# Performance work log

Hardware: AMD Instinct MI355X
Metric: run time of the kernel (lower is better)

Reference implementation:

```python
import jax, jax.numpy as jnp
import numpy as np

B, H, W, C, WS, NH = 32, 56, 56, 384, 7, 12
HD = C // NH            # head dim = 32
HID = 4 * C             # mlp hidden = 1536
SCALE = HD ** -0.5
EPS = 1e-5


def setup_inputs() -> dict:
    key = jax.random.key(0)
    ks = jax.random.split(key, 12)
    w = lambda k, shape: jax.random.normal(k, shape, jnp.float32) * 0.02
    return {
        "x": jax.random.normal(ks[0], (B, H * W, C), jnp.float32),
        "ln1_w": jnp.ones((C,), jnp.float32),
        "ln1_b": jnp.zeros((C,), jnp.float32),
        "qkv_w": w(ks[1], (3 * C, C)),          # nn.Linear weight [out,in], no bias
        "proj_w": w(ks[2], (C, C)),
        "proj_b": jnp.zeros((C,), jnp.float32),
        "ln2_w": jnp.ones((C,), jnp.float32),
        "ln2_b": jnp.zeros((C,), jnp.float32),
        "fc1_w": w(ks[3], (HID, C)),
        "fc1_b": jnp.zeros((HID,), jnp.float32),
        "fc2_w": w(ks[4], (C, HID)),
        "fc2_b": jnp.zeros((C,), jnp.float32),
    }


def _layer_norm(x, w, b):
    mu = jnp.mean(x, axis=-1, keepdims=True)
    var = jnp.mean((x - mu) ** 2, axis=-1, keepdims=True)
    return (x - mu) * jax.lax.rsqrt(var + EPS) * w + b


def _window_partition(x):
    # x: [B, H, W, C] -> [B*nW, WS*WS, C]
    x = x.reshape(B, H // WS, WS, W // WS, WS, C)
    x = x.transpose(0, 1, 3, 2, 4, 5)
    return x.reshape(-1, WS * WS, C)


def _window_reverse(xw):
    # [B*nW, WS*WS, C] -> [B, H*W, C]
    x = xw.reshape(B, H // WS, W // WS, WS, WS, C)
    x = x.transpose(0, 1, 3, 2, 4, 5)
    return x.reshape(B, H * W, C)


def reference(x, ln1_w, ln1_b, qkv_w, proj_w, proj_b, ln2_w, ln2_b,
              fc1_w, fc1_b, fc2_w, fc2_b):
    h = x
    xn = _layer_norm(x, ln1_w, ln1_b)
    xw = _window_partition(xn.reshape(B, H, W, C))      # [nB, N, C], N = 49

    # windowed multi-head self-attention
    qkv = xw @ qkv_w.T                                  # [nB, N, 3C]
    q, k, v = jnp.split(qkv, 3, axis=-1)
    def heads(t):
        return t.reshape(t.shape[0], t.shape[1], NH, HD).transpose(0, 2, 1, 3)
    q, k, v = heads(q), heads(k), heads(v)              # [nB, NH, N, HD]
    attn = jnp.einsum('bhnd,bhmd->bhnm', q, k) * SCALE
    attn = jax.nn.softmax(attn, axis=-1)
    out = jnp.einsum('bhnm,bhmd->bhnd', attn, v)        # [nB, NH, N, HD]
    out = out.transpose(0, 2, 1, 3).reshape(xw.shape[0], WS * WS, C)
    out = out @ proj_w.T + proj_b

    x = h + _window_reverse(out)

    # MLP (note: GELU applied after both fc1 and fc2, as in source)
    h = x
    xn = _layer_norm(x, ln2_w, ln2_b)
    y = jax.nn.gelu(xn @ fc1_w.T + fc1_b, approximate=False)
    y = jax.nn.gelu(y @ fc2_w.T + fc2_b, approximate=False)
    return h + y
```

## Files before the change

kernel.cpp:

```cpp
#include <hip/hip_runtime.h>
#include <cstdint>

#define TOKENS 100352
#define CDIM 384
#define HIDDIM 1536
#define NQKV 1152
#define NHEAD 12
#define NWIN_ALL 2048

typedef __bf16 bf16x8 __attribute__((ext_vector_type(8)));
typedef float f32x4 __attribute__((ext_vector_type(4)));
typedef unsigned short u16;
typedef u16 u16x8 __attribute__((ext_vector_type(8)));

typedef __attribute__((address_space(1))) unsigned int u32_as1;
typedef __attribute__((address_space(3))) unsigned int u32_as3;

__device__ __forceinline__ float bf2f(u16 u) {
    union { unsigned int i; float f; } v; v.i = ((unsigned int)u) << 16; return v.f;
}
__device__ __forceinline__ u16 f2bf(float f) {
    union { float f; unsigned int i; } v; v.f = f;
    unsigned int i = v.i;
    i += 0x7fffu + ((i >> 16) & 1u);
    return (u16)(i >> 16);
}
__device__ __forceinline__ float gelu_f(float x) {
    const float u = x * (0.7978845608028654f + 0.035677408136300125f * x * x);
    const float a = __builtin_fabsf(u);
    const float e = __expf(2.0f * a);
    float t = 1.0f - 2.0f * __builtin_amdgcn_rcpf(e + 1.0f);
    t = __builtin_copysignf(t, u);
    return 0.5f * x * (1.0f + t);
}
__device__ __forceinline__ void gload16(const u16* g, u16* l) {
    __builtin_amdgcn_global_load_lds((const u32_as1*)g, (u32_as3*)l, 16, 0, 0);
}

__global__ void cvt_kernel(const float* __restrict__ in, u16* __restrict__ out, int n) {
    int i = blockIdx.x * blockDim.x + threadIdx.x;
    if (i < n) out[i] = f2bf(in[i]);
}

__global__ __launch_bounds__(256) void ln_kernel(const float* __restrict__ x,
                                                 const float* __restrict__ w,
                                                 const float* __restrict__ b,
                                                 u16* __restrict__ out) {
    const int wid = threadIdx.x >> 6, lane = threadIdx.x & 63;
    const long row = (long)blockIdx.x * 4 + wid;
    const float* xr = x + row * CDIM;
    float v[6];
#pragma unroll
    for (int i = 0; i < 6; i++) v[i] = xr[lane + i * 64];
    float s = 0.f;
#pragma unroll
    for (int i = 0; i < 6; i++) s += v[i];
#pragma unroll
    for (int off = 32; off >= 1; off >>= 1) s += __shfl_xor(s, off, 64);
    const float mu = s * (1.0f / CDIM);
    float q = 0.f;
#pragma unroll
    for (int i = 0; i < 6; i++) { float d = v[i] - mu; q += d * d; }
#pragma unroll
    for (int off = 32; off >= 1; off >>= 1) q += __shfl_xor(q, off, 64);
    const float rs = rsqrtf(q * (1.0f / CDIM) + 1e-5f);
    u16* orow = out + row * CDIM;
#pragma unroll
    for (int i = 0; i < 6; i++) {
        const int c = lane + i * 64;
        orow[c] = f2bf((v[i] - mu) * rs * w[c] + b[c]);
    }
}

template <int EPI>
__global__ __launch_bounds__(256, 2) void gemm_kernel(const u16* __restrict__ A,
                                                      const u16* __restrict__ Bw,
                                                      const float* __restrict__ bias,
                                                      const float* __restrict__ res,
                                                      void* __restrict__ outp,
                                                      int N, int K) {
    __shared__ u16 lsA0[128 * 64];
    __shared__ u16 lsB0[128 * 64];
    __shared__ u16 lsA1[128 * 64];
    __shared__ u16 lsB1[128 * 64];
    const int ntiles = N >> 7;
    const int nwg = gridDim.x;
    const int bid = blockIdx.x;
    const int wg = ((nwg & 7) == 0) ? ((bid & 7) * (nwg >> 3) + (bid >> 3)) : bid;
    const int tm = wg / ntiles, tn = wg % ntiles;
    const int tid = threadIdx.x, wid = tid >> 6, lane = tid & 63;
    const int wr = wid >> 1, wc = wid & 1;

    const int srow = wid * 32 + (lane >> 3);
    const int schunk = (lane & 7) ^ (lane >> 3);
    const u16* gA = A + (size_t)(tm * 128 + srow) * K + schunk * 8;
    const u16* gB = Bw + (size_t)(tn * 128 + srow) * K + schunk * 8;
    const size_t rskip = (size_t)8 * K;
    const int lofs = wid * 2048;

    f32x4 acc[4][4] = {};

    const int rA = wr * 64 + (lane & 15);
    const int rB = wc * 64 + (lane & 15);
    const int ksub = lane >> 4;
    const int rx = lane & 7;

    auto STAGE = [&](u16* la, u16* lb, int kofs) {
#pragma unroll
        for (int j = 0; j < 4; j++) {
            gload16(gA + kofs + j * rskip, la + lofs + j * 512);
            gload16(gB + kofs + j * rskip, lb + lofs + j * 512);
        }
    };
    auto COMPUTE = [&](const u16* la, const u16* lb) {
#pragma unroll
        for (int kk = 0; kk < 2; kk++) {
            const int ca = (((kk << 2) + ksub) ^ rx) << 3;
            bf16x8 af[4], bfr[4];
#pragma unroll
            for (int mi = 0; mi < 4; mi++)
                af[mi] = *(const bf16x8*)(la + (rA + mi * 16) * 64 + ca);
#pragma unroll
            for (int ni = 0; ni < 4; ni++)
                bfr[ni] = *(const bf16x8*)(lb + (rB + ni * 16) * 64 + ca);
#pragma unroll
            for (int mi = 0; mi < 4; mi++)
#pragma unroll
                for (int ni = 0; ni < 4; ni++)
                    acc[mi][ni] = __builtin_amdgcn_mfma_f32_16x16x32_bf16(af[mi], bfr[ni], acc[mi][ni], 0, 0, 0);
        }
    };

    STAGE(lsA0, lsB0, 0);
    __syncthreads();
    const int nt = K >> 6;
    for (int t = 0; t < nt; t += 2) {
        STAGE(lsA1, lsB1, (t + 1) << 6);
        COMPUTE(lsA0, lsB0);
        __syncthreads();
        if (t + 2 < nt) STAGE(lsA0, lsB0, (t + 2) << 6);
        COMPUTE(lsA1, lsB1);
        __syncthreads();
    }

    const int r0 = tm * 128 + wr * 64 + ((lane >> 4) << 2);
    const int c0 = tn * 128 + wc * 64 + (lane & 15);
#pragma unroll
    for (int ni = 0; ni < 4; ni++) {
        const int col = c0 + ni * 16;
        const float bc = (EPI == 0) ? 0.0f : bias[col];
#pragma unroll
        for (int mi = 0; mi < 4; mi++) {
#pragma unroll
            for (int r = 0; r < 4; r++) {
                const size_t row = (size_t)(r0 + mi * 16 + r);
                const size_t idx = row * (size_t)N + col;
                const float v = acc[mi][ni][r];
                if (EPI == 1)      ((float*)outp)[idx] = v + bc + res[idx];
                else if (EPI == 2) ((u16*)outp)[idx] = f2bf(gelu_f(v + bc));
                else if (EPI == 3) ((float*)outp)[idx] = res[idx] + gelu_f(v + bc);
                else               ((u16*)outp)[idx] = f2bf(v);
            }
        }
    }
}

__global__ __launch_bounds__(64) void attn_kernel(const u16* __restrict__ qkv,
                                                  u16* __restrict__ out) {
    const int blk = blockIdx.x;
    const int head = blk % NHEAD;
    const int win = blk / NHEAD;
    const int b = win >> 6, wy = (win >> 3) & 7, wx = win & 7;
    const int lane = threadIdx.x;
    const int base_tok = b * 3136 + wy * 7 * 56 + wx * 7;

    __shared__ float kf[49][32];
    __shared__ float vf[49][32];

    for (int ci = lane; ci < 392; ci += 64) {
        const int which = ci >= 196;
        const int c = which ? ci - 196 : ci;
        const int row = c >> 2, sub = c & 3;
        const int t = base_tok + (row / 7) * 56 + (row % 7);
        const u16* src = qkv + (size_t)t * NQKV + (which ? 768 : 384) + head * 32 + sub * 8;
        const u16x8 u = *(const u16x8*)src;
        float* dst = (which ? vf[row] : kf[row]) + sub * 8;
#pragma unroll
        for (int j = 0; j < 8; j++) dst[j] = bf2f(u[j]);
    }
    __syncthreads();

    if (lane < 49) {
        const int t = base_tok + (lane / 7) * 56 + (lane % 7);
        const u16* qsrc = qkv + (size_t)t * NQKV + head * 32;
        float qr[32];
#pragma unroll
        for (int sub = 0; sub < 4; sub++) {
            const u16x8 u = *(const u16x8*)(qsrc + sub * 8);
#pragma unroll
            for (int j = 0; j < 8; j++) qr[sub * 8 + j] = bf2f(u[j]) * 0.17677669529663688f;
        }
        float s[49];
        float mx = -1e30f;
#pragma unroll
        for (int m = 0; m < 49; m++) {
            float a = 0.f;
#pragma unroll
            for (int d = 0; d < 32; d++) a += qr[d] * kf[m][d];
            s[m] = a; mx = fmaxf(mx, a);
        }
        float sum = 0.f;
#pragma unroll
        for (int m = 0; m < 49; m++) { const float e = expf(s[m] - mx); s[m] = e; sum += e; }
        const float inv = 1.0f / sum;
        float o[32];
#pragma unroll
        for (int d = 0; d < 32; d++) o[d] = 0.f;
#pragma unroll
        for (int m = 0; m < 49; m++) {
            const float p = s[m] * inv;
#pragma unroll
            for (int d = 0; d < 32; d++) o[d] += p * vf[m][d];
        }
        u16* dst = out + (size_t)t * CDIM + head * 32;
#pragma unroll
        for (int sub = 0; sub < 4; sub++) {
            u16x8 u;
#pragma unroll
            for (int j = 0; j < 8; j++) u[j] = f2bf(o[sub * 8 + j]);
            *(u16x8*)(dst + sub * 8) = u;
        }
    }
}

extern "C" void kernel_launch(void* const* d_in, const int* in_sizes, int n_in,
                              void* d_out, int out_size, void* d_ws, size_t ws_size,
                              hipStream_t stream) {
    const float* x     = (const float*)d_in[0];
    const float* ln1w  = (const float*)d_in[1];
    const float* ln1b  = (const float*)d_in[2];
    const float* qkvw  = (const float*)d_in[3];
    const float* projw = (const float*)d_in[4];
    const float* projb = (const float*)d_in[5];
    const float* ln2w  = (const float*)d_in[6];
    const float* ln2b  = (const float*)d_in[7];
    const float* fc1w  = (const float*)d_in[8];
    const float* fc1b  = (const float*)d_in[9];
    const float* fc2w  = (const float*)d_in[10];
    const float* fc2b  = (const float*)d_in[11];
    float* out = (float*)d_out;

    const size_t sz_xn = (size_t)TOKENS * CDIM * 2;
    const size_t sz_w  = ((size_t)NQKV * CDIM + (size_t)CDIM * CDIM +
                          (size_t)HIDDIM * CDIM + (size_t)CDIM * HIDDIM) * 2;
    if (sz_xn + sz_w > ws_size) return;
    const size_t avail = ws_size - sz_xn - sz_w;

    int nc_a = 1;
    while (nc_a <= 32 && (size_t)(TOKENS / nc_a) * NQKV * 2 > avail) nc_a <<= 1;
    int nc_m = 1;
    while (nc_m <= 16 && (size_t)(TOKENS / nc_m) * HIDDIM * 2 > avail) nc_m <<= 1;
    if (nc_a > 32 || nc_m > 16) return;

    char* ws = (char*)d_ws;
    u16* xn   = (u16*)ws;  ws += sz_xn;
    u16* wq = (u16*)ws; ws += (size_t)NQKV * CDIM * 2;
    u16* wp = (u16*)ws; ws += (size_t)CDIM * CDIM * 2;
    u16* w1 = (u16*)ws; ws += (size_t)HIDDIM * CDIM * 2;
    u16* w2 = (u16*)ws; ws += (size_t)CDIM * HIDDIM * 2;
    u16* cbuf = (u16*)ws;

    cvt_kernel<<<(NQKV * CDIM + 255) / 256, 256, 0, stream>>>(qkvw, wq, NQKV * CDIM);
    cvt_kernel<<<(CDIM * CDIM + 255) / 256, 256, 0, stream>>>(projw, wp, CDIM * CDIM);
    cvt_kernel<<<(HIDDIM * CDIM + 255) / 256, 256, 0, stream>>>(fc1w, w1, HIDDIM * CDIM);
    cvt_kernel<<<(CDIM * HIDDIM + 255) / 256, 256, 0, stream>>>(fc2w, w2, CDIM * HIDDIM);

    ln_kernel<<<TOKENS / 4, 256, 0, stream>>>(x, ln1w, ln1b, xn);

    {
        const int ctok = TOKENS / nc_a;
        for (int c = 0; c < nc_a; c++) {
            u16* xnc = xn + (size_t)c * ctok * CDIM;
            gemm_kernel<0><<<(ctok / 128) * (NQKV / 128), 256, 0, stream>>>(
                xnc, wq, nullptr, nullptr, cbuf, NQKV, CDIM);
            attn_kernel<<<(NWIN_ALL / nc_a) * NHEAD, 64, 0, stream>>>(cbuf, xnc);
        }
    }

    gemm_kernel<1><<<(TOKENS / 128) * (CDIM / 128), 256, 0, stream>>>(
        xn, wp, projb, x, out, CDIM, CDIM);

    ln_kernel<<<TOKENS / 4, 256, 0, stream>>>(out, ln2w, ln2b, xn);

    {
        const int ctok = TOKENS / nc_m;
        for (int c = 0; c < nc_m; c++) {
            const u16* xnc = xn + (size_t)c * ctok * CDIM;
            float* outc = out + (size_t)c * ctok * CDIM;
            gemm_kernel<2><<<(ctok / 128) * (HIDDIM / 128), 256, 0, stream>>>(
                xnc, w1, fc1b, nullptr, cbuf, HIDDIM, CDIM);
            gemm_kernel<3><<<(ctok / 128) * (CDIM / 128), 256, 0, stream>>>(
                cbuf, w2, fc2b, outc, outc, CDIM, HIDDIM);
        }
    }
}
```

Before: 1.256 ms.

## Rewrite window attention with MFMA bf16 matrix ops, one wave per window-head

Replaces the scalar per-lane attention (49 active lanes computing dot products against fp32 K/V in LDS) with MFMA 16x16x32 bf16 instructions. Q·K^T and P·V are tiled into 16x16 blocks padded to 64 tokens. Softmax runs on the accumulator fragments with cross-lane shuffles and exp2, and P is staged in swizzled LDS. Each 256-thread block now handles four window-head pairs, one per wave. This removes the heavy scalar FMA work and the idle lanes, at the cost of padding waste and extra bf16 rounding of the probabilities.

```diff
diff --git a/kernel.cpp b/kernel.cpp
--- a/kernel.cpp
+++ b/kernel.cpp
@@ -165,72 +165,128 @@
     }
 }
 
-__global__ __launch_bounds__(64) void attn_kernel(const u16* __restrict__ qkv,
-                                                  u16* __restrict__ out) {
-    const int blk = blockIdx.x;
-    const int head = blk % NHEAD;
-    const int win = blk / NHEAD;
+__global__ __launch_bounds__(256, 4) void attn_kernel(const u16* __restrict__ qkv,
+                                                      u16* __restrict__ out) {
+    __shared__ u16 pbuf[4 * 64 * 64];
+    const int wid = threadIdx.x >> 6, lane = threadIdx.x & 63;
+    const int id = blockIdx.x * 4 + wid;
+    const int head = id % NHEAD;
+    const int win = id / NHEAD;
     const int b = win >> 6, wy = (win >> 3) & 7, wx = win & 7;
-    const int lane = threadIdx.x;
-    const int base_tok = b * 3136 + wy * 7 * 56 + wx * 7;
-
-    __shared__ float kf[49][32];
-    __shared__ float vf[49][32];
-
-    for (int ci = lane; ci < 392; ci += 64) {
-        const int which = ci >= 196;
-        const int c = which ? ci - 196 : ci;
-        const int row = c >> 2, sub = c & 3;
-        const int t = base_tok + (row / 7) * 56 + (row % 7);
-        const u16* src = qkv + (size_t)t * NQKV + (which ? 768 : 384) + head * 32 + sub * 8;
-        const u16x8 u = *(const u16x8*)src;
-        float* dst = (which ? vf[row] : kf[row]) + sub * 8;
-#pragma unroll
-        for (int j = 0; j < 8; j++) dst[j] = bf2f(u[j]);
-    }
-    __syncthreads();
-
-    if (lane < 49) {
-        const int t = base_tok + (lane / 7) * 56 + (lane % 7);
-        const u16* qsrc = qkv + (size_t)t * NQKV + head * 32;
-        float qr[32];
-#pragma unroll
-        for (int sub = 0; sub < 4; sub++) {
-            const u16x8 u = *(const u16x8*)(qsrc + sub * 8);
-#pragma unroll
-            for (int j = 0; j < 8; j++) qr[sub * 8 + j] = bf2f(u[j]) * 0.17677669529663688f;
-        }
-        float s[49];
-        float mx = -1e30f;
-#pragma unroll
-        for (int m = 0; m < 49; m++) {
-            float a = 0.f;
-#pragma unroll
-            for (int d = 0; d < 32; d++) a += qr[d] * kf[m][d];
-            s[m] = a; mx = fmaxf(mx, a);
-        }
-        float sum = 0.f;
-#pragma unroll
-        for (int m = 0; m < 49; m++) { const float e = expf(s[m] - mx); s[m] = e; sum += e; }
-        const float inv = 1.0f / sum;
-        float o[32];
-#pragma unroll
-        for (int d = 0; d < 32; d++) o[d] = 0.f;
-#pragma unroll
-        for (int m = 0; m < 49; m++) {
-            const float p = s[m] * inv;
-#pragma unroll
-            for (int d = 0; d < 32; d++) o[d] += p * vf[m][d];
-        }
-        u16* dst = out + (size_t)t * CDIM + head * 32;
-#pragma unroll
-        for (int sub = 0; sub < 4; sub++) {
-            u16x8 u;
-#pragma unroll
-            for (int j = 0; j < 8; j++) u[j] = f2bf(o[sub * 8 + j]);
-            *(u16x8*)(dst + sub * 8) = u;
-        }
-    }
+    const int base_tok = b * 3136 + wy * 392 + wx * 7;
+    const int l15 = lane & 15, lg = lane >> 4;
+    u16* pw = pbuf + wid * 4096;
+
+    bf16x8 qf[4], kf[4];
+#pragma unroll
+    for (int t4 = 0; t4 < 4; t4++) {
+        const int r = t4 * 16 + l15;
+        if (r < 49) {
+            const size_t to = (size_t)(base_tok + (r / 7) * 56 + (r % 7)) * NQKV + head * 32 + lg * 8;
+            qf[t4] = *(const bf16x8*)(qkv + to);
+            kf[t4] = *(const bf16x8*)(qkv + to + 384);
+        } else {
+#pragma unroll
+            for (int j = 0; j < 8; j++) { qf[t4][j] = (__bf16)0.0f; kf[t4][j] = (__bf16)0.0f; }
+        }
+    }
+
+    f32x4 s[4][4] = {};
+#pragma unroll
+    for (int qt = 0; qt < 4; qt++)
+#pragma unroll
+        for (int nt = 0; nt < 4; nt++)
+            s[qt][nt] = __builtin_amdgcn_mfma_f32_16x16x32_bf16(qf[qt], kf[nt], s[qt][nt], 0, 0, 0);
+
+    const float NEG = -1e30f;
+    if (l15 >= 1) {
+#pragma unroll
+        for (int qt = 0; qt < 4; qt++)
+#pragma unroll
+            for (int r = 0; r < 4; r++) s[qt][3][r] = NEG;
+    }
+    float rm[4][4], inv[4][4];
+#pragma unroll
+    for (int qt = 0; qt < 4; qt++)
+#pragma unroll
+        for (int r = 0; r < 4; r++) {
+            float m = fmaxf(fmaxf(s[qt][0][r], s[qt][1][r]), fmaxf(s[qt][2][r], s[qt][3][r]));
+#pragma unroll
+            for (int off = 1; off <= 8; off <<= 1) m = fmaxf(m, __shfl_xor(m, off, 64));
+            rm[qt][r] = m;
+        }
+    const float cexp = 0.25508682f;
+#pragma unroll
+    for (int qt = 0; qt < 4; qt++)
+#pragma unroll
+        for (int nt = 0; nt < 4; nt++)
+#pragma unroll
+            for (int r = 0; r < 4; r++)
+                s[qt][nt][r] = exp2f((s[qt][nt][r] - rm[qt][r]) * cexp);
+#pragma unroll
+    for (int qt = 0; qt < 4; qt++)
+#pragma unroll
+        for (int r = 0; r < 4; r++) {
+            float su = s[qt][0][r] + s[qt][1][r] + s[qt][2][r] + s[qt][3][r];
+#pragma unroll
+            for (int off = 1; off <= 8; off <<= 1) su += __shfl_xor(su, off, 64);
+            inv[qt][r] = 1.0f / su;
+        }
+
+#pragma unroll
+    for (int qt = 0; qt < 4; qt++)
+#pragma unroll
+        for (int nt = 0; nt < 4; nt++)
+#pragma unroll
+            for (int r = 0; r < 4; r++) {
+                const int row = qt * 16 + lg * 4 + r;
+                const int col = nt * 16 + l15;
+                pw[row * 64 + (((col >> 3) ^ (row & 7)) << 3) + (col & 7)] = f2bf(s[qt][nt][r]);
+            }
+
+    u16x8 vtu[2][2];
+#pragma unroll
+    for (int ks = 0; ks < 2; ks++)
+#pragma unroll
+        for (int j = 0; j < 8; j++) {
+            const int k = ks * 32 + lg * 8 + j;
+            u16 v0 = 0, v1 = 0;
+            if (k < 49) {
+                const size_t to = (size_t)(base_tok + (k / 7) * 56 + (k % 7)) * NQKV + 768 + head * 32 + l15;
+                v0 = qkv[to]; v1 = qkv[to + 16];
+            }
+            vtu[0][ks][j] = v0; vtu[1][ks][j] = v1;
+        }
+
+    f32x4 oa[4][2] = {};
+#pragma unroll
+    for (int ks = 0; ks < 2; ks++) {
+        bf16x8 pa[4];
+#pragma unroll
+        for (int qt = 0; qt < 4; qt++) {
+            const int row = qt * 16 + l15;
+            pa[qt] = *(const bf16x8*)(pw + row * 64 + (((ks * 4 + lg) ^ (row & 7)) << 3));
+        }
+#pragma unroll
+        for (int qt = 0; qt < 4; qt++)
+#pragma unroll
+            for (int dt = 0; dt < 2; dt++)
+                oa[qt][dt] = __builtin_amdgcn_mfma_f32_16x16x32_bf16(
+                    pa[qt], *(const bf16x8*)&vtu[dt][ks], oa[qt][dt], 0, 0, 0);
+    }
+
+#pragma unroll
+    for (int qt = 0; qt < 4; qt++)
+#pragma unroll
+        for (int r = 0; r < 4; r++) {
+            const int row = qt * 16 + lg * 4 + r;
+            if (row < 49) {
+                const int t = base_tok + (row / 7) * 56 + (row % 7);
+                u16* dst = out + (size_t)t * CDIM + head * 32 + l15;
+                dst[0]  = f2bf(oa[qt][0][r] * inv[qt][r]);
+                dst[16] = f2bf(oa[qt][1][r] * inv[qt][r]);
+            }
+        }
 }
 
 extern "C" void kernel_launch(void* const* d_in, const int* in_sizes, int n_in,
@@ -279,11 +335,12 @@
 
     {
         const int ctok = TOKENS / nc_a;
+        const int cwin = NWIN_ALL / nc_a;
         for (int c = 0; c < nc_a; c++) {
             u16* xnc = xn + (size_t)c * ctok * CDIM;
             gemm_kernel<0><<<(ctok / 128) * (NQKV / 128), 256, 0, stream>>>(
                 xnc, wq, nullptr, nullptr, cbuf, NQKV, CDIM);
-            attn_kernel<<<(NWIN_ALL / nc_a) * NHEAD, 64, 0, stream>>>(cbuf, xnc);
+            attn_kernel<<<(cwin * NHEAD) / 4, 256, 0, stream>>>(cbuf, xnc);
         }
     }
 
```

Measured after the change: 1.096 ms. -12.7%, faster.
